# Kernel tuning notes

Hardware: AMD Instinct MI355X
Metric: run time of the kernel (lower is better)

## Reference

```python
import jax, jax.numpy as jnp
import numpy as np

EMBED_DIM = 1280
NUM_HEADS = 20
HEAD_DIM = EMBED_DIM // NUM_HEADS  # 64
TGT_LEN = 2048
BSZ = 2
SCALING = HEAD_DIM ** -0.5


def setup_inputs() -> dict:
    key = jax.random.key(0)
    ks = jax.random.split(key, 6)
    s = EMBED_DIM ** -0.5
    query = jax.random.normal(ks[0], (TGT_LEN, BSZ, EMBED_DIM), dtype=jnp.float32)
    Wq = jax.random.normal(ks[1], (EMBED_DIM, EMBED_DIM), dtype=jnp.float32) * s
    Wk = jax.random.normal(ks[2], (EMBED_DIM, EMBED_DIM), dtype=jnp.float32) * s
    Wv = jax.random.normal(ks[3], (EMBED_DIM, EMBED_DIM), dtype=jnp.float32) * s
    Wo = jax.random.normal(ks[4], (EMBED_DIM, EMBED_DIM), dtype=jnp.float32) * s
    bq = jnp.zeros((EMBED_DIM,), jnp.float32)
    bk = jnp.zeros((EMBED_DIM,), jnp.float32)
    bv = jnp.zeros((EMBED_DIM,), jnp.float32)
    bo = jnp.zeros((EMBED_DIM,), jnp.float32)
    # key_padding_mask: (bsz, src_len), True = padded; pad last 256 keys of batch 1
    kpm = np.zeros((BSZ, TGT_LEN), dtype=bool)
    kpm[1, -256:] = True
    key_padding_mask = jnp.asarray(kpm)
    return {"query": query, "key_padding_mask": key_padding_mask,
            "Wq": Wq, "bq": bq, "Wk": Wk, "bk": bk,
            "Wv": Wv, "bv": bv, "Wo": Wo, "bo": bo}


def _mha(query, key_padding_mask, Wq, bq, Wk, bk, Wv, bv, Wo, bo):
    T, B, E = query.shape
    H, D = NUM_HEADS, HEAD_DIM
    q = (query @ Wq + bq) * SCALING            # [T, B, E]
    k = query @ Wk + bk
    v = query @ Wv + bv
    # reshape to [B*H, T, D] as in the TF code
    q = q.reshape(T, B * H, D).transpose(1, 0, 2)
    k = k.reshape(T, B * H, D).transpose(1, 0, 2)
    v = v.reshape(T, B * H, D).transpose(1, 0, 2)
    attn_weights = jnp.einsum('bqd,bkd->bqk', q, k)   # [B*H, T, T]
    # key padding mask: (B, src_len), 1s excluded -> -inf
    aw = attn_weights.reshape(B, H, T, T)
    aw = jnp.where(key_padding_mask[:, None, None, :], -jnp.inf, aw)
    attn_weights_float = jax.nn.softmax(aw.astype(jnp.float32).reshape(B * H, T, T), axis=-1)
    attn_probs = attn_weights_float.astype(v.dtype)  # dropout rate 0.0 -> identity
    attn = jnp.einsum('bqk,bkd->bqd', attn_probs, v)  # [B*H, T, D]
    attn = attn.transpose(1, 0, 2).reshape(T, B, E)
    attn = attn @ Wo + bo
    # need_weights=True (default), need_head_weights=False -> mean over heads
    avg_weights = attn_weights_float.reshape(B, H, T, T).transpose(1, 0, 2, 3).mean(axis=0)
    return attn, avg_weights


def reference(query, key_padding_mask, Wq, bq, Wk, bk, Wv, bv, Wo, bo):
    return _mha(query, key_padding_mask, Wq, bq, Wk, bk, Wv, bv, Wo, bo)
```

## Files before the change

### kernel.cpp

```cpp
#include <hip/hip_runtime.h>

#define T_LEN 2048
#define BSZ   2
#define EMB   1280
#define NH    20
#define HD    64
#define NBH   (BSZ*NH)
#define NR    (T_LEN*BSZ)
#define QSCALE (0.125f * 1.4426950408889634f)

#define KPAD 68

typedef short bf16x8 __attribute__((ext_vector_type(8)));
typedef short bf16x4 __attribute__((ext_vector_type(4)));
typedef float f32x4  __attribute__((ext_vector_type(4)));

__device__ inline short f2bf(float f) {
    union { float f; unsigned u; } v; v.f = f;
    unsigned u = v.u + 0x7FFF + ((v.u >> 16) & 1);
    return (short)(u >> 16);
}

__device__ inline unsigned cvt_pk_bf16(float lo, float hi) {
    unsigned r;
    asm("v_cvt_pk_bf16_f32 %0, %1, %2" : "=v"(r) : "v"(lo), "v"(hi));
    return r;
}

__device__ inline void glds16(const short* g, short* l) {
    __builtin_amdgcn_global_load_lds(
        (const __attribute__((address_space(1))) void*)g,
        (__attribute__((address_space(3))) void*)l,
        16, 0, 0);
}

__global__ __launch_bounds__(256) void k_cvt_x(
    const float* __restrict__ X, short* __restrict__ Xb)
{
    size_t i0 = ((size_t)blockIdx.x*256 + threadIdx.x) * 8;
    float4 a = *(const float4*)(X + i0);
    float4 b = *(const float4*)(X + i0 + 4);
    bf16x8 r = { f2bf(a.x), f2bf(a.y), f2bf(a.z), f2bf(a.w),
                 f2bf(b.x), f2bf(b.y), f2bf(b.z), f2bf(b.w) };
    *(bf16x8*)(Xb + i0) = r;
}

__global__ __launch_bounds__(256) void k_cvt_wt(
    const float* __restrict__ Wq, const float* __restrict__ Wk,
    const float* __restrict__ Wv, const float* __restrict__ Wo,
    short* __restrict__ Wqt, short* __restrict__ Wkt,
    short* __restrict__ Wvt, short* __restrict__ Wot)
{
    const int z = blockIdx.z;
    const float* __restrict__ W = (z==0)?Wq:(z==1)?Wk:(z==2)?Wv:Wo;
    short* __restrict__ Wt      = (z==0)?Wqt:(z==1)?Wkt:(z==2)?Wvt:Wot;

    const int k0 = blockIdx.y * 32;
    const int n0 = blockIdx.x * 32;
    const int t  = threadIdx.x;

    __shared__ float Ls[32][33];
    {
        int row = t >> 3, col = (t & 7) * 4;
        *(float4*)&Ls[row][col] = *(const float4*)(W + (size_t)(k0+row)*EMB + n0 + col);
    }
    __syncthreads();
    {
        int n = t >> 3, k4 = (t & 7) * 4;
        bf16x4 r = { f2bf(Ls[k4+0][n]), f2bf(Ls[k4+1][n]),
                     f2bf(Ls[k4+2][n]), f2bf(Ls[k4+3][n]) };
        *(bf16x4*)(Wt + (size_t)(n0+n)*EMB + k0 + k4) = r;
    }
}

__global__ __launch_bounds__(256) void k_gemm_qkv(
    const short* __restrict__ Xb,
    const short* __restrict__ Wqt, const short* __restrict__ Wkt, const short* __restrict__ Wvt,
    const float* __restrict__ bq, const float* __restrict__ bk, const float* __restrict__ bv,
    short* __restrict__ Qb, short* __restrict__ Kb, short* __restrict__ Vt)
{
    const int which = blockIdx.z;
    const short* __restrict__ Wt   = (which==0) ? Wqt : (which==1) ? Wkt : Wvt;
    const float* __restrict__ bias = (which==0) ? bq  : (which==1) ? bk  : bv;
    const float scale = (which==0) ? QSCALE : 1.0f;

    const int bm = blockIdx.y * 128;
    const int bn = blockIdx.x * 128;
    const int t    = threadIdx.x;
    const int wave = t >> 6, lane = t & 63;
    const int l16  = lane & 15, quad = lane >> 4;
    const int wm   = (wave >> 1) * 64, wn = (wave & 1) * 64;

    __shared__ short As[128][64];
    __shared__ short Bs[128][64];

    const int srow   = lane >> 3;
    const int scolsw = (((lane & 7) ^ srow) & 7) * 8;
    const int rsw    = (l16 & 7) << 3;

    f32x4 acc[4][4] = {};

    for (int kt = 0; kt < EMB; kt += 64) {
        __syncthreads();
        const short* Ag = Xb + (size_t)bm*EMB + kt;
        const short* Bg = Wt + (size_t)bn*EMB + kt;
        #pragma unroll
        for (int c = 0; c < 4; ++c) {
            int seg = wave*4 + c;
            int grow = seg*8 + srow;
            glds16(Ag + (size_t)grow*EMB + scolsw, &As[seg*8][0]);
            glds16(Bg + (size_t)grow*EMB + scolsw, &Bs[seg*8][0]);
        }
        __syncthreads();
        #pragma unroll
        for (int ks = 0; ks < 64; ks += 32) {
            bf16x8 af[4], bfr[4];
            #pragma unroll
            for (int mi=0;mi<4;++mi) af[mi]  = *(const bf16x8*)&As[wm + mi*16 + l16][(ks + quad*8) ^ rsw];
            #pragma unroll
            for (int ni=0;ni<4;++ni) bfr[ni] = *(const bf16x8*)&Bs[wn + ni*16 + l16][(ks + quad*8) ^ rsw];
            #pragma unroll
            for (int mi=0;mi<4;++mi)
                #pragma unroll
                for (int ni=0;ni<4;++ni)
                    acc[mi][ni] = __builtin_amdgcn_mfma_f32_16x16x32_bf16(af[mi], bfr[ni], acc[mi][ni], 0,0,0);
        }
    }

    #pragma unroll
    for (int ni=0;ni<4;++ni) {
        int c = bn + wn + ni*16 + l16;
        float bval = bias[c];
        int h = c >> 6, d = c & 63;
        #pragma unroll
        for (int mi=0;mi<4;++mi) {
            #pragma unroll
            for (int j=0;j<4;++j) {
                int r = bm + wm + mi*16 + quad*4 + j;
                int tt = r >> 1, bb = r & 1;
                float val = (acc[mi][ni][j] + bval) * scale;
                if (which == 2)
                    Vt[((size_t)(bb*NH+h)*HD + d)*T_LEN + tt] = f2bf(val);
                else {
                    short* dst = (which==0) ? Qb : Kb;
                    dst[((size_t)(bb*NH+h)*T_LEN + tt)*HD + d] = f2bf(val);
                }
            }
        }
    }
}

__global__ __launch_bounds__(512) void k_pv(
    const short* __restrict__ Qb, const short* __restrict__ Kb, const short* __restrict__ Vt,
    const int* __restrict__ kpm,
    float* __restrict__ Linv,
    short* __restrict__ AttnMidb)
{
    int lin = blockIdx.y*gridDim.x + blockIdx.x;
    lin = (lin & 7) * 80 + (lin >> 3);
    const int qt = lin & 15;
    const int bh = lin >> 4;
    const int b  = bh / NH, h = bh % NH;
    const int t    = threadIdx.x;
    const int w    = t >> 6;
    const int lane = t & 63;
    const int l16  = lane & 15;
    const int quad = lane >> 4;
    const int q0   = qt*128 + w*16;

    __shared__ short Ks[2][64][KPAD];
    __shared__ short Vts[2][64][KPAD];
    __shared__ float MfL[2][64];
    __shared__ float Lsh[128];

    bf16x8 qf[2];
    #pragma unroll
    for (int ch=0;ch<2;++ch)
        qf[ch] = *(const bf16x8*)(Qb + ((size_t)bh*T_LEN + q0 + l16)*HD + ch*32 + quad*8);

    const int row0 = t >> 3, col8 = (t & 7) * 8;
    const short* Kgb = Kb + (size_t)bh*T_LEN*HD;
    const short* Vgb = Vt + (size_t)bh*HD*T_LEN;

    *(bf16x8*)&Ks[0][row0][col8]  = *(const bf16x8*)(Kgb + (size_t)row0*HD + col8);
    *(bf16x8*)&Vts[0][row0][col8] = *(const bf16x8*)(Vgb + (size_t)row0*T_LEN + col8);
    if (t < 64) MfL[0][t] = kpm[b*T_LEN + t] ? 0.f : 1.f;
    __syncthreads();

    f32x4 o[4] = {};
    float l = 0.f;
    int cur = 0;

    for (int kt = 0; kt < T_LEN; kt += 64) {
        const int ktn = kt + 64;
        const bool has_next = ktn < T_LEN;
        const int nxt = cur ^ 1;

        bf16x8 kr0, vr0;
        float mfn = 0.f;
        if (has_next) {
            kr0 = *(const bf16x8*)(Kgb + (size_t)(ktn + row0)*HD + col8);
            vr0 = *(const bf16x8*)(Vgb + (size_t)row0*T_LEN + ktn + col8);
            if (t < 64) mfn = kpm[b*T_LEN + ktn + t] ? 0.f : 1.f;
        }

        f32x4 s[4] = {};
        #pragma unroll
        for (int ch = 0; ch < 2; ++ch) {
            bf16x8 ka[4];
            #pragma unroll
            for (int mb=0;mb<4;++mb) ka[mb] = *(const bf16x8*)&Ks[cur][mb*16 + l16][ch*32 + quad*8];
            #pragma unroll
            for (int mb=0;mb<4;++mb)
                s[mb] = __builtin_amdgcn_mfma_f32_16x16x32_bf16(ka[mb], qf[ch], s[mb], 0,0,0);
        }

        unsigned pu[2][4];
        #pragma unroll
        for (int c = 0; c < 2; ++c) {
            #pragma unroll
            for (int mb2 = 0; mb2 < 2; ++mb2) {
                const int mb = c*2 + mb2;
                float4 mf = *(const float4*)&MfL[cur][mb*16 + quad*4];
                float p0 = __builtin_amdgcn_exp2f(s[mb][0]) * mf.x;
                float p1 = __builtin_amdgcn_exp2f(s[mb][1]) * mf.y;
                float p2 = __builtin_amdgcn_exp2f(s[mb][2]) * mf.z;
                float p3 = __builtin_amdgcn_exp2f(s[mb][3]) * mf.w;
                l += (p0 + p1) + (p2 + p3);
                pu[c][mb2*2+0] = cvt_pk_bf16(p0, p1);
                pu[c][mb2*2+1] = cvt_pk_bf16(p2, p3);
            }
        }

        if (has_next) {
            *(bf16x8*)&Ks[nxt][row0][col8]  = kr0;
            *(bf16x8*)&Vts[nxt][row0][col8] = vr0;
            if (t < 64) MfL[nxt][t] = mfn;
        }

        #pragma unroll
        for (int c = 0; c < 2; ++c) {
            bf16x8 vv[4];
            #pragma unroll
            for (int nb=0;nb<4;++nb) {
                bf16x4 va = *(const bf16x4*)&Vts[cur][nb*16 + l16][c*32 + quad*4];
                bf16x4 vb = *(const bf16x4*)&Vts[cur][nb*16 + l16][c*32 + 16 + quad*4];
                vv[nb] = (bf16x8){va[0],va[1],va[2],va[3], vb[0],vb[1],vb[2],vb[3]};
            }
            union { unsigned u[4]; bf16x8 v; } pa;
            pa.u[0]=pu[c][0]; pa.u[1]=pu[c][1];
            pa.u[2]=pu[c][2]; pa.u[3]=pu[c][3];
            #pragma unroll
            for (int nb=0;nb<4;++nb)
                o[nb] = __builtin_amdgcn_mfma_f32_16x16x32_bf16(pa.v, vv[nb], o[nb], 0,0,0);
        }

        __syncthreads();
        cur = nxt;
    }

    l += __shfl_xor(l, 16);
    l += __shfl_xor(l, 32);
    float linv = 1.0f / l;
    if (quad == 0) {
        Linv[(size_t)bh*T_LEN + q0 + l16] = linv;
        Lsh[w*16 + l16] = linv;
    }
    {
        float4 li = *(const float4*)&Lsh[w*16 + quad*4];
        float lr[4] = {li.x, li.y, li.z, li.w};
        #pragma unroll
        for (int r=0;r<4;++r) {
            int q = q0 + quad*4 + r;
            size_t base = ((size_t)q*BSZ + b)*EMB + h*HD;
            #pragma unroll
            for (int nb=0;nb<4;++nb)
                AttnMidb[base + nb*16 + l16] = f2bf(o[nb][r] * lr[r]);
        }
    }
}

__global__ __launch_bounds__(256) void k_meanw(
    const short* __restrict__ Qb, const short* __restrict__ Kb,
    const int* __restrict__ kpm,
    const float* __restrict__ Linv,
    float* __restrict__ avg)
{
    int lin = (blockIdx.z*gridDim.y + blockIdx.y)*gridDim.x + blockIdx.x;
    lin = (lin & 7) * 256 + (lin >> 3);
    const int kt = lin & 31;
    const int qt = (lin >> 5) & 31;
    const int b  = lin >> 10;

    const int t    = threadIdx.x;
    const int wave = t >> 6, lane = t & 63;
    const int l16  = lane & 15, quad = lane >> 4;

    __shared__ short Qs[2][64][KPAD];
    __shared__ short Ks[2][64][KPAD];
    __shared__ float Lish[2][64];
    __shared__ int   msk[64];

    const int srow = t >> 2;
    const int scol = (t & 3) * 16;

    const short* Qg0 = Qb + ((size_t)(b*NH)*T_LEN + qt*64)*HD;
    const short* Kg0 = Kb + ((size_t)(b*NH)*T_LEN + kt*64)*HD;
    const size_t hstride = (size_t)T_LEN*HD;

    if (t < 64) msk[t] = kpm[b*T_LEN + kt*64 + t];

    *(bf16x8*)&Qs[0][srow][scol]   = *(const bf16x8*)(Qg0 + (size_t)srow*HD + scol);
    *(bf16x8*)&Qs[0][srow][scol+8] = *(const bf16x8*)(Qg0 + (size_t)srow*HD + scol + 8);
    *(bf16x8*)&Ks[0][srow][scol]   = *(const bf16x8*)(Kg0 + (size_t)srow*HD + scol);
    *(bf16x8*)&Ks[0][srow][scol+8] = *(const bf16x8*)(Kg0 + (size_t)srow*HD + scol + 8);
    if (t < 64) Lish[0][t] = Linv[(size_t)(b*NH)*T_LEN + qt*64 + t];
    __syncthreads();

    f32x4 acc[4] = {};
    const int qrow_in = wave*16 + quad*4;
    int cur = 0;

    for (int h = 0; h < NH; ++h) {
        const int nxt = cur ^ 1;

        bf16x8 qr0, qr1, kr0, kr1;
        float lnx = 0.f;
        if (h+1 < NH) {
            const short* Qg = Qg0 + (size_t)(h+1)*hstride;
            const short* Kg = Kg0 + (size_t)(h+1)*hstride;
            qr0 = *(const bf16x8*)(Qg + (size_t)srow*HD + scol);
            qr1 = *(const bf16x8*)(Qg + (size_t)srow*HD + scol + 8);
            kr0 = *(const bf16x8*)(Kg + (size_t)srow*HD + scol);
            kr1 = *(const bf16x8*)(Kg + (size_t)srow*HD + scol + 8);
            if (t < 64) lnx = Linv[(size_t)(b*NH + h+1)*T_LEN + qt*64 + t];
        }

        bf16x8 aq0 = *(const bf16x8*)&Qs[cur][wave*16 + l16][quad*8];
        bf16x8 aq1 = *(const bf16x8*)&Qs[cur][wave*16 + l16][32 + quad*8];

        float lv[4];
        #pragma unroll
        for (int r = 0; r < 4; ++r)
            lv[r] = Lish[cur][qrow_in + r] * (1.0f/NH);

        #pragma unroll
        for (int nb = 0; nb < 4; ++nb) {
            bf16x8 bk0 = *(const bf16x8*)&Ks[cur][nb*16 + l16][quad*8];
            bf16x8 bk1 = *(const bf16x8*)&Ks[cur][nb*16 + l16][32 + quad*8];
            f32x4 s = {};
            s = __builtin_amdgcn_mfma_f32_16x16x32_bf16(aq0, bk0, s, 0,0,0);
            s = __builtin_amdgcn_mfma_f32_16x16x32_bf16(aq1, bk1, s, 0,0,0);
            const bool mk = msk[nb*16 + l16] != 0;
            #pragma unroll
            for (int r = 0; r < 4; ++r)
                acc[nb][r] += mk ? 0.f : __builtin_amdgcn_exp2f(s[r]) * lv[r];
        }

        if (h+1 < NH) {
            *(bf16x8*)&Qs[nxt][srow][scol]   = qr0;
            *(bf16x8*)&Qs[nxt][srow][scol+8] = qr1;
            *(bf16x8*)&Ks[nxt][srow][scol]   = kr0;
            *(bf16x8*)&Ks[nxt][srow][scol+8] = kr1;
            if (t < 64) Lish[nxt][t] = lnx;
        }
        __syncthreads();
        cur = nxt;
    }

    #pragma unroll
    for (int r = 0; r < 4; ++r) {
        int q = qt*64 + qrow_in + r;
        size_t base = ((size_t)b*T_LEN + q) * T_LEN + (size_t)kt*64;
        #pragma unroll
        for (int nb = 0; nb < 4; ++nb)
            avg[base + nb*16 + l16] = acc[nb][r];
    }
}

__global__ __launch_bounds__(256) void k_gemm_out(
    const short* __restrict__ Ab, const short* __restrict__ Wot,
    const float* __restrict__ bo, float* __restrict__ out)
{
    const int bm = blockIdx.y * 128;
    const int bn = blockIdx.x * 128;
    const int t    = threadIdx.x;
    const int wave = t >> 6, lane = t & 63;
    const int l16  = lane & 15, quad = lane >> 4;
    const int wm   = (wave >> 1) * 64, wn = (wave & 1) * 64;

    __shared__ short As[128][64];
    __shared__ short Bs[128][64];

    const int srow   = lane >> 3;
    const int scolsw = (((lane & 7) ^ srow) & 7) * 8;
    const int rsw    = (l16 & 7) << 3;

    f32x4 acc[4][4] = {};

    for (int kt = 0; kt < EMB; kt += 64) {
        __syncthreads();
        const short* Ag = Ab  + (size_t)bm*EMB + kt;
        const short* Bg = Wot + (size_t)bn*EMB + kt;
        #pragma unroll
        for (int c = 0; c < 4; ++c) {
            int seg = wave*4 + c;
            int grow = seg*8 + srow;
            glds16(Ag + (size_t)grow*EMB + scolsw, &As[seg*8][0]);
            glds16(Bg + (size_t)grow*EMB + scolsw, &Bs[seg*8][0]);
        }
        __syncthreads();
        #pragma unroll
        for (int ks = 0; ks < 64; ks += 32) {
            bf16x8 af[4], bfr[4];
            #pragma unroll
            for (int mi=0;mi<4;++mi) af[mi]  = *(const bf16x8*)&As[wm + mi*16 + l16][(ks + quad*8) ^ rsw];
            #pragma unroll
            for (int ni=0;ni<4;++ni) bfr[ni] = *(const bf16x8*)&Bs[wn + ni*16 + l16][(ks + quad*8) ^ rsw];
            #pragma unroll
            for (int mi=0;mi<4;++mi)
                #pragma unroll
                for (int ni=0;ni<4;++ni)
                    acc[mi][ni] = __builtin_amdgcn_mfma_f32_16x16x32_bf16(af[mi], bfr[ni], acc[mi][ni], 0,0,0);
        }
    }

    #pragma unroll
    for (int ni=0;ni<4;++ni) {
        int c = bn + wn + ni*16 + l16;
        float bval = bo[c];
        #pragma unroll
        for (int mi=0;mi<4;++mi) {
            #pragma unroll
            for (int j=0;j<4;++j) {
                int r = bm + wm + mi*16 + quad*4 + j;
                out[(size_t)r*EMB + c] = acc[mi][ni][j] + bval;
            }
        }
    }
}

extern "C" void kernel_launch(void* const* d_in, const int* in_sizes, int n_in,
                              void* d_out, int out_size, void* d_ws, size_t ws_size,
                              hipStream_t stream) {
    const float* X   = (const float*)d_in[0];
    const int*   kpm = (const int*)  d_in[1];
    const float* Wq  = (const float*)d_in[2];
    const float* bq  = (const float*)d_in[3];
    const float* Wk  = (const float*)d_in[4];
    const float* bk  = (const float*)d_in[5];
    const float* Wv  = (const float*)d_in[6];
    const float* bv  = (const float*)d_in[7];
    const float* Wo  = (const float*)d_in[8];
    const float* bo  = (const float*)d_in[9];

    float* out = (float*)d_out;
    float* ws  = (float*)d_ws;

    const size_t QKV = (size_t)NBH * T_LEN * HD;
    float* Linv = ws;
    short* Xb   = (short*)(Linv + (size_t)NBH * T_LEN);
    short* Wqt  = Xb  + (size_t)NR * EMB;
    short* Wkt  = Wqt + (size_t)EMB * EMB;
    short* Wvt  = Wkt + (size_t)EMB * EMB;
    short* Wot  = Wvt + (size_t)EMB * EMB;
    short* Qb   = Wot + (size_t)EMB * EMB;
    short* Kb   = Qb  + QKV;
    short* Vt   = Kb  + QKV;
    short* Amid = Vt  + QKV;

    float* attn_out = out;
    float* avg      = out + (size_t)T_LEN * BSZ * EMB;

    k_cvt_x   <<<dim3((NR*EMB)/(256*8)), 256, 0, stream>>>(X, Xb);
    k_cvt_wt  <<<dim3(EMB/32, EMB/32, 4), 256, 0, stream>>>(Wq, Wk, Wv, Wo, Wqt, Wkt, Wvt, Wot);
    k_gemm_qkv<<<dim3(EMB/128, NR/128, 3), 256, 0, stream>>>(Xb, Wqt, Wkt, Wvt, bq, bk, bv, Qb, Kb, Vt);
    k_pv      <<<dim3(T_LEN/128, NBH),   512, 0, stream>>>(Qb, Kb, Vt, kpm, Linv, Amid);
    k_meanw   <<<dim3(T_LEN/64, T_LEN/64, BSZ), 256, 0, stream>>>(Qb, Kb, kpm, Linv, avg);
    k_gemm_out<<<dim3(EMB/128, NR/128),  256, 0, stream>>>(Amid, Wot, bo, attn_out);
}
```

Before: 341.4 us.

## Remap GEMM block order for XCD locality and load Q directly to registers

The QKV and output-projection GEMMs now remap the linear block index so that consecutive blocks on each XCD (assigned round-robin across 8) share row stripes and weight columns, aiming for better L2 reuse. In the mean-weights kernel, each wave loads its own 16 Q rows straight from global memory into registers and prefetches the next head's Q the same way. This drops the Q shared-memory tile and its LDS traffic. The trade-off is smaller, less coalesced per-lane global Q loads, and the remap hardcodes the grid sizes.

```diff
diff --git a/kernel.cpp b/kernel.cpp
--- a/kernel.cpp
+++ b/kernel.cpp
@@ -79,13 +79,19 @@
     const float* __restrict__ bq, const float* __restrict__ bk, const float* __restrict__ bv,
     short* __restrict__ Qb, short* __restrict__ Kb, short* __restrict__ Vt)
 {
-    const int which = blockIdx.z;
+    int orig = (blockIdx.z*gridDim.y + blockIdx.y)*gridDim.x + blockIdx.x;
+    int wp = (orig & 7)*120 + (orig >> 3);
+    const int bm2    = wp & 1;
+    const int bnn    = (wp >> 1) % 10;
+    const int stripe = (wp / 20) & 15;
+    const int which  = wp / 320;
+
     const short* __restrict__ Wt   = (which==0) ? Wqt : (which==1) ? Wkt : Wvt;
     const float* __restrict__ bias = (which==0) ? bq  : (which==1) ? bk  : bv;
     const float scale = (which==0) ? QSCALE : 1.0f;
 
-    const int bm = blockIdx.y * 128;
-    const int bn = blockIdx.x * 128;
+    const int bm = (stripe*2 + bm2) * 128;
+    const int bn = bnn * 128;
     const int t    = threadIdx.x;
     const int wave = t >> 6, lane = t & 63;
     const int l16  = lane & 15, quad = lane >> 4;
@@ -296,7 +302,6 @@
     const int wave = t >> 6, lane = t & 63;
     const int l16  = lane & 15, quad = lane >> 4;
 
-    __shared__ short Qs[2][64][KPAD];
     __shared__ short Ks[2][64][KPAD];
     __shared__ float Lish[2][64];
     __shared__ int   msk[64];
@@ -304,17 +309,17 @@
     const int srow = t >> 2;
     const int scol = (t & 3) * 16;
 
-    const short* Qg0 = Qb + ((size_t)(b*NH)*T_LEN + qt*64)*HD;
     const short* Kg0 = Kb + ((size_t)(b*NH)*T_LEN + kt*64)*HD;
+    const short* Qf  = Qb + ((size_t)(b*NH)*T_LEN + qt*64 + wave*16 + l16)*HD;
     const size_t hstride = (size_t)T_LEN*HD;
 
     if (t < 64) msk[t] = kpm[b*T_LEN + kt*64 + t];
 
-    *(bf16x8*)&Qs[0][srow][scol]   = *(const bf16x8*)(Qg0 + (size_t)srow*HD + scol);
-    *(bf16x8*)&Qs[0][srow][scol+8] = *(const bf16x8*)(Qg0 + (size_t)srow*HD + scol + 8);
     *(bf16x8*)&Ks[0][srow][scol]   = *(const bf16x8*)(Kg0 + (size_t)srow*HD + scol);
     *(bf16x8*)&Ks[0][srow][scol+8] = *(const bf16x8*)(Kg0 + (size_t)srow*HD + scol + 8);
     if (t < 64) Lish[0][t] = Linv[(size_t)(b*NH)*T_LEN + qt*64 + t];
+    bf16x8 aq0 = *(const bf16x8*)(Qf + quad*8);
+    bf16x8 aq1 = *(const bf16x8*)(Qf + 32 + quad*8);
     __syncthreads();
 
     f32x4 acc[4] = {};
@@ -324,20 +329,17 @@
     for (int h = 0; h < NH; ++h) {
         const int nxt = cur ^ 1;
 
-        bf16x8 qr0, qr1, kr0, kr1;
+        bf16x8 kr0, kr1, qn0, qn1;
         float lnx = 0.f;
         if (h+1 < NH) {
-            const short* Qg = Qg0 + (size_t)(h+1)*hstride;
             const short* Kg = Kg0 + (size_t)(h+1)*hstride;
-            qr0 = *(const bf16x8*)(Qg + (size_t)srow*HD + scol);
-            qr1 = *(const bf16x8*)(Qg + (size_t)srow*HD + scol + 8);
             kr0 = *(const bf16x8*)(Kg + (size_t)srow*HD + scol);
             kr1 = *(const bf16x8*)(Kg + (size_t)srow*HD + scol + 8);
+            const short* Qh = Qf + (size_t)(h+1)*hstride;
+            qn0 = *(const bf16x8*)(Qh + quad*8);
+            qn1 = *(const bf16x8*)(Qh + 32 + quad*8);
             if (t < 64) lnx = Linv[(size_t)(b*NH + h+1)*T_LEN + qt*64 + t];
         }
-
-        bf16x8 aq0 = *(const bf16x8*)&Qs[cur][wave*16 + l16][quad*8];
-        bf16x8 aq1 = *(const bf16x8*)&Qs[cur][wave*16 + l16][32 + quad*8];
 
         float lv[4];
         #pragma unroll
@@ -358,11 +360,10 @@
         }
 
         if (h+1 < NH) {
-            *(bf16x8*)&Qs[nxt][srow][scol]   = qr0;
-            *(bf16x8*)&Qs[nxt][srow][scol+8] = qr1;
             *(bf16x8*)&Ks[nxt][srow][scol]   = kr0;
             *(bf16x8*)&Ks[nxt][srow][scol+8] = kr1;
             if (t < 64) Lish[nxt][t] = lnx;
+            aq0 = qn0; aq1 = qn1;
         }
         __syncthreads();
         cur = nxt;
@@ -382,8 +383,14 @@
     const short* __restrict__ Ab, const short* __restrict__ Wot,
     const float* __restrict__ bo, float* __restrict__ out)
 {
-    const int bm = blockIdx.y * 128;
-    const int bn = blockIdx.x * 128;
+    int orig = blockIdx.y*gridDim.x + blockIdx.x;
+    int wp = (orig & 7)*40 + (orig >> 3);
+    const int bm2    = wp & 1;
+    const int bnn    = (wp >> 1) % 10;
+    const int stripe = wp / 20;
+
+    const int bm = (stripe*2 + bm2) * 128;
+    const int bn = bnn * 128;
     const int t    = threadIdx.x;
     const int wave = t >> 6, lane = t & 63;
     const int l16  = lane & 15, quad = lane >> 4;
```

Result: no change. 347.5 us (+1.8%).
